# Kernel optimization log

Measured on AMD Instinct MI355X. Metric: run time of the kernel, lower is better.

## Reference

```python
import jax, jax.numpy as jnp
import numpy as np

N = 50000      # nodes (cells)
E = 800000     # directed edges
IN, H1, H2, Z = 512, 128, 128, 64


def setup_inputs() -> dict:
    key = jax.random.key(0)
    ks = jax.random.split(key, 12)
    x = jax.random.normal(ks[0], (N, IN), jnp.float32)
    edge_index = jax.random.randint(ks[1], (2, E), 0, N, dtype=jnp.int64)

    def glorot(k, i, o):
        return jax.random.normal(k, (i, o), jnp.float32) * np.float32(1.0 / np.sqrt(i))

    return {
        "x": x,
        "edge_index": edge_index,
        "W1": glorot(ks[2], IN, H1), "b1": jnp.zeros((H1,), jnp.float32),
        "W2": glorot(ks[3], H1, H2), "b2": jnp.zeros((H2,), jnp.float32),
        "Wm": glorot(ks[4], H2, Z),  "bm": jnp.zeros((Z,), jnp.float32),
        "Ws": glorot(ks[5], H2, Z),  "bs": jnp.zeros((Z,), jnp.float32),
    }


def _gcn_norm(edge_index, n):
    # PyG GCNConv default: add self-loops, sym-normalize D^-1/2 (A+I) D^-1/2
    loops = jnp.arange(n, dtype=edge_index.dtype)
    src = jnp.concatenate([edge_index[0], loops])
    dst = jnp.concatenate([edge_index[1], loops])
    deg = jax.ops.segment_sum(jnp.ones_like(dst, jnp.float32), dst, num_segments=n)
    dis = jnp.where(deg > 0, jax.lax.rsqrt(jnp.maximum(deg, 1.0)), 0.0)
    norm = dis[src] * dis[dst]  # [E+N]
    return src, dst, norm


def _gcn_conv(x, W, b, src, dst, norm, n):
    h = x @ W                          # [N, out] transform first
    msg = h[src] * norm[:, None]       # gather + scale
    out = jax.ops.segment_sum(msg, dst, num_segments=n)  # scatter-add at targets
    return out + b


def reference(x, edge_index, W1, b1, W2, b2, Wm, bm, Ws, bs):
    n = x.shape[0]
    src, dst, norm = _gcn_norm(edge_index, n)
    h = jax.nn.relu(_gcn_conv(x, W1, b1, src, dst, norm, n))
    h = jax.nn.relu(_gcn_conv(h, W2, b2, src, dst, norm, n))
    # dropout p=0.4 is identity in eval mode
    z_mean = _gcn_conv(h, Wm, bm, src, dst, norm, n)
    z_log_std = _gcn_conv(h, Ws, bs, src, dst, norm, n)
    return (z_mean, z_log_std)
```

## Files before the change

### kernel.cpp

```cpp
#include <hip/hip_runtime.h>


using u16 = unsigned short;
typedef __attribute__((ext_vector_type(8))) short short8;
typedef __attribute__((ext_vector_type(4))) float f32x4;

__device__ __forceinline__ void split_bf16(float f, u16& hi, u16& lo) {
    unsigned b = __float_as_uint(f);
    hi = (u16)(b >> 16);
    float rem = f - __uint_as_float(b & 0xFFFF0000u);
    lo = (u16)(__float_as_uint(rem) >> 16);
}

__device__ __forceinline__ int block_mode(const int* __restrict__ ew, int* sflag) {
    if (threadIdx.x == 0) *sflag = 0;
    __syncthreads();
    if (ew[2 * (int)threadIdx.x + 1] != 0) atomicOr(sflag, 1);
    __syncthreads();
    return *sflag ? 0 : 1;
}

__global__ void deg_kernel(const int* __restrict__ ew, int* __restrict__ deg, int E) {
    __shared__ int sflag;
    int mode = block_mode(ew, &sflag);
    int e = blockIdx.x * blockDim.x + threadIdx.x;
    if (e >= E) return;
    int d = mode ? ew[2 * E + 2 * e] : ew[E + e];
    atomicAdd(&deg[d], 1);
}

__global__ void scan_block_kernel(const int* __restrict__ deg, int* __restrict__ rowptr,
                                  int* __restrict__ aux, float* __restrict__ dis, int N) {
    __shared__ int s[256];
    int i = blockIdx.x * 256 + threadIdx.x;
    int v = (i < N) ? deg[i] : 0;
    if (i < N) dis[i] = rsqrtf((float)v + 1.0f);
    s[threadIdx.x] = v;
    __syncthreads();
    for (int off = 1; off < 256; off <<= 1) {
        int t = (threadIdx.x >= off) ? s[threadIdx.x - off] : 0;
        __syncthreads();
        s[threadIdx.x] += t;
        __syncthreads();
    }
    if (i < N) rowptr[i] = s[threadIdx.x] - v;
    if (threadIdx.x == 255) aux[blockIdx.x] = s[255];
}

__global__ void scan_aux_kernel(int* __restrict__ aux, int nb) {
    __shared__ int s[256];
    int i = threadIdx.x;
    int v = (i < nb) ? aux[i] : 0;
    s[i] = v;
    __syncthreads();
    for (int off = 1; off < 256; off <<= 1) {
        int t = (i >= off) ? s[i - off] : 0;
        __syncthreads();
        s[i] += t;
        __syncthreads();
    }
    if (i < nb) aux[i] = s[i] - v;
}

__global__ void add_offsets_kernel(int* __restrict__ rowptr, const int* __restrict__ aux,
                                   int N, int E) {
    int i = blockIdx.x * 256 + threadIdx.x;
    if (i < N) rowptr[i] += aux[i >> 8];
    if (i == 0) rowptr[N] = E;
}

__global__ void fill_csr_kernel(const int* __restrict__ ew,
                                const int* __restrict__ rowptr, int* __restrict__ cursor,
                                int* __restrict__ csr_src, int E) {
    __shared__ int sflag;
    int mode = block_mode(ew, &sflag);
    int e = blockIdx.x * blockDim.x + threadIdx.x;
    if (e >= E) return;
    int s = mode ? ew[2 * e] : ew[e];
    int d = mode ? ew[2 * E + 2 * e] : ew[E + e];
    int pos = rowptr[d] + atomicAdd(&cursor[d], 1);
    csr_src[pos] = s;
}

__global__ void conv_all_kernel(const float* __restrict__ W1, const float* __restrict__ W2,
                                const float* __restrict__ Wm, const float* __restrict__ Ws,
                                u16* __restrict__ W1t_hi, u16* __restrict__ W1t_lo,
                                u16* __restrict__ W2t_hi, u16* __restrict__ W2t_lo,
                                u16* __restrict__ Wct_hi, u16* __restrict__ Wct_lo) {
    int idx = blockIdx.x * 256 + threadIdx.x;
    u16 h, l;
    if (idx < 65536) {
        int k = idx >> 7, n = idx & 127;
        split_bf16(W1[idx], h, l);
        W1t_hi[n * 512 + k] = h;
        W1t_lo[n * 512 + k] = l;
    } else if (idx < 81920) {
        int t = idx - 65536;
        int k = t >> 7, n = t & 127;
        split_bf16(W2[t], h, l);
        W2t_hi[n * 128 + k] = h;
        W2t_lo[n * 128 + k] = l;
    } else if (idx < 98304) {
        int t = idx - 81920;
        int k = t >> 7, j = t & 127;
        float f = (j < 64) ? Wm[k * 64 + j] : Ws[k * 64 + (j - 64)];
        split_bf16(f, h, l);
        Wct_hi[j * 128 + k] = h;
        Wct_lo[j * 128 + k] = l;
    }
}

#define TILE_OFF(t) ((t) * 520)

__global__ __launch_bounds__(256) void gemm_mfma(const float* __restrict__ A,
                                                 const u16* __restrict__ Bt_hi,
                                                 const u16* __restrict__ Bt_lo,
                                                 float* __restrict__ C,
                                                 int N, int K) {
    __shared__ u16 AsH[4 * 520], AsL[4 * 520];
    __shared__ u16 BsH[8 * 520], BsL[8 * 520];

    const int tid = threadIdx.x;
    const int w = tid >> 6, lane = tid & 63;
    const int row0 = blockIdx.y * 64;

    const int s_ar = w * 16 + (lane & 15);
    const int s_ak = (lane >> 4) * 8;
    const int a_dst = TILE_OFF(w) + lane * 8;
    const int s_bc = tid >> 1;
    const int s_bk = (tid & 1) * 16;
    const int b_q0 = (tid & 1) * 2;
    const int b_dst0 = TILE_OFF(s_bc >> 4) + ((s_bc & 15) + 16 * (b_q0 + 0)) * 8;
    const int b_dst1 = TILE_OFF(s_bc >> 4) + ((s_bc & 15) + 16 * (b_q0 + 1)) * 8;

    const int R = (w >> 1) * 32, Cc = (w & 1) * 64;
    const int atile = (w >> 1) * 2;
    const int btile = (w & 1) * 4;
    const int m16 = lane & 15, quad = lane >> 4;

    f32x4 acc[2][4];
#pragma unroll
    for (int i = 0; i < 2; ++i)
#pragma unroll
        for (int j = 0; j < 4; ++j) acc[i][j] = (f32x4)0.f;

    const int grow = row0 + s_ar;
    const bool ok = (grow < N);
    const float* aptr = A + (size_t)grow * K + s_ak;
    const u16* bph = Bt_hi + (size_t)s_bc * K + s_bk;
    const u16* bpl = Bt_lo + (size_t)s_bc * K + s_bk;

    float av[8];
    short8 rbh0, rbh1, rbl0, rbl1;
    {
        f32x4 v0 = (f32x4)0.f, v1 = (f32x4)0.f;
        if (ok) { v0 = *(const f32x4*)&aptr[0]; v1 = *(const f32x4*)&aptr[4]; }
#pragma unroll
        for (int q = 0; q < 4; ++q) { av[q] = v0[q]; av[4 + q] = v1[q]; }
        rbh0 = *(const short8*)&bph[0];
        rbh1 = *(const short8*)&bph[8];
        rbl0 = *(const short8*)&bpl[0];
        rbl1 = *(const short8*)&bpl[8];
    }

    const int ksteps = K >> 5;
    for (int ks = 0; ks < ksteps; ++ks) {
        short8 ah, al;
#pragma unroll
        for (int q = 0; q < 8; ++q) {
            u16 h, l;
            split_bf16(av[q], h, l);
            ah[q] = (short)h;
            al[q] = (short)l;
        }
        __syncthreads();
        *(short8*)&AsH[a_dst] = ah;
        *(short8*)&AsL[a_dst] = al;
        *(short8*)&BsH[b_dst0] = rbh0;
        *(short8*)&BsH[b_dst1] = rbh1;
        *(short8*)&BsL[b_dst0] = rbl0;
        *(short8*)&BsL[b_dst1] = rbl1;
        __syncthreads();

        if (ks + 1 < ksteps) {
            const int k0 = (ks + 1) * 32;
            f32x4 v0 = (f32x4)0.f, v1 = (f32x4)0.f;
            if (ok) { v0 = *(const f32x4*)&aptr[k0]; v1 = *(const f32x4*)&aptr[k0 + 4]; }
#pragma unroll
            for (int q = 0; q < 4; ++q) { av[q] = v0[q]; av[4 + q] = v1[q]; }
            rbh0 = *(const short8*)&bph[k0];
            rbh1 = *(const short8*)&bph[k0 + 8];
            rbl0 = *(const short8*)&bpl[k0];
            rbl1 = *(const short8*)&bpl[k0 + 8];
        }

        short8 fa_h[2], fa_l[2], fb_h[4], fb_l[4];
#pragma unroll
        for (int i = 0; i < 2; ++i) {
            fa_h[i] = *(const short8*)&AsH[TILE_OFF(atile + i) + lane * 8];
            fa_l[i] = *(const short8*)&AsL[TILE_OFF(atile + i) + lane * 8];
        }
#pragma unroll
        for (int j = 0; j < 4; ++j) {
            fb_h[j] = *(const short8*)&BsH[TILE_OFF(btile + j) + lane * 8];
            fb_l[j] = *(const short8*)&BsL[TILE_OFF(btile + j) + lane * 8];
        }
#pragma unroll
        for (int i = 0; i < 2; ++i)
#pragma unroll
            for (int j = 0; j < 4; ++j) {
                acc[i][j] = __builtin_amdgcn_mfma_f32_16x16x32_bf16(
                    fa_h[i], fb_h[j], acc[i][j], 0, 0, 0);
                acc[i][j] = __builtin_amdgcn_mfma_f32_16x16x32_bf16(
                    fa_h[i], fb_l[j], acc[i][j], 0, 0, 0);
                acc[i][j] = __builtin_amdgcn_mfma_f32_16x16x32_bf16(
                    fa_l[i], fb_h[j], acc[i][j], 0, 0, 0);
            }
    }

#pragma unroll
    for (int i = 0; i < 2; ++i) {
#pragma unroll
        for (int r = 0; r < 4; ++r) {
            int gr = row0 + R + i * 16 + quad * 4 + r;
            if (gr < N) {
#pragma unroll
                for (int j = 0; j < 4; ++j)
                    C[(size_t)gr * 128 + Cc + j * 16 + m16] = acc[i][j][r];
            }
        }
    }
}

__global__ __launch_bounds__(256) void propagate_kernel(
    const float* __restrict__ h, const int* __restrict__ rowptr,
    const int* __restrict__ csr_src, const float* __restrict__ dis,
    const float* __restrict__ bias, float* __restrict__ out, int N, int do_relu) {
    int wave = (blockIdx.x * 256 + threadIdx.x) >> 6;
    int lane = threadIdx.x & 63;
    if (wave >= N) return;
    int v = wave;
    int f = lane * 2;
    float dv = dis[v];
    float ax = 0.f, ay = 0.f;
    int beg = rowptr[v], end = rowptr[v + 1];
    int i = beg;
    for (; i + 8 <= end; i += 8) {
        int s[8];
        float ww[8];
        float2 g[8];
#pragma unroll
        for (int u = 0; u < 8; ++u) s[u] = csr_src[i + u];
#pragma unroll
        for (int u = 0; u < 8; ++u) ww[u] = dis[s[u]];
#pragma unroll
        for (int u = 0; u < 8; ++u) g[u] = *(const float2*)&h[(size_t)s[u] * 128 + f];
#pragma unroll
        for (int u = 0; u < 8; ++u) {
            float t = ww[u] * dv;
            ax += t * g[u].x;
            ay += t * g[u].y;
        }
    }
    if (i + 4 <= end) {
        int s[4];
        float ww[4];
        float2 g[4];
#pragma unroll
        for (int u = 0; u < 4; ++u) s[u] = csr_src[i + u];
#pragma unroll
        for (int u = 0; u < 4; ++u) ww[u] = dis[s[u]];
#pragma unroll
        for (int u = 0; u < 4; ++u) g[u] = *(const float2*)&h[(size_t)s[u] * 128 + f];
#pragma unroll
        for (int u = 0; u < 4; ++u) {
            float t = ww[u] * dv;
            ax += t * g[u].x;
            ay += t * g[u].y;
        }
        i += 4;
    }
    for (; i < end; ++i) {
        int s = csr_src[i];
        float ws = dis[s] * dv;
        float2 g = *(const float2*)&h[(size_t)s * 128 + f];
        ax += ws * g.x;
        ay += ws * g.y;
    }
    float2 hv = *(const float2*)&h[(size_t)v * 128 + f];
    ax += dv * dv * hv.x;
    ay += dv * dv * hv.y;
    ax += bias[f];
    ay += bias[f + 1];
    if (do_relu) { ax = fmaxf(ax, 0.f); ay = fmaxf(ay, 0.f); }
    *(float2*)&out[(size_t)v * 128 + f] = make_float2(ax, ay);
}

__global__ __launch_bounds__(256) void propagate_final_kernel(
    const float* __restrict__ h, const int* __restrict__ rowptr,
    const int* __restrict__ csr_src, const float* __restrict__ dis,
    const float* __restrict__ bm, const float* __restrict__ bs,
    float* __restrict__ out, int N) {
    int wave = (blockIdx.x * 256 + threadIdx.x) >> 6;
    int lane = threadIdx.x & 63;
    if (wave >= N) return;
    int v = wave;
    int f = lane * 2;
    float dv = dis[v];
    float ax = 0.f, ay = 0.f;
    int beg = rowptr[v], end = rowptr[v + 1];
    int i = beg;
    for (; i + 8 <= end; i += 8) {
        int s[8];
        float ww[8];
        float2 g[8];
#pragma unroll
        for (int u = 0; u < 8; ++u) s[u] = csr_src[i + u];
#pragma unroll
        for (int u = 0; u < 8; ++u) ww[u] = dis[s[u]];
#pragma unroll
        for (int u = 0; u < 8; ++u) g[u] = *(const float2*)&h[(size_t)s[u] * 128 + f];
#pragma unroll
        for (int u = 0; u < 8; ++u) {
            float t = ww[u] * dv;
            ax += t * g[u].x;
            ay += t * g[u].y;
        }
    }
    if (i + 4 <= end) {
        int s[4];
        float ww[4];
        float2 g[4];
#pragma unroll
        for (int u = 0; u < 4; ++u) s[u] = csr_src[i + u];
#pragma unroll
        for (int u = 0; u < 4; ++u) ww[u] = dis[s[u]];
#pragma unroll
        for (int u = 0; u < 4; ++u) g[u] = *(const float2*)&h[(size_t)s[u] * 128 + f];
#pragma unroll
        for (int u = 0; u < 4; ++u) {
            float t = ww[u] * dv;
            ax += t * g[u].x;
            ay += t * g[u].y;
        }
        i += 4;
    }
    for (; i < end; ++i) {
        int s = csr_src[i];
        float ws = dis[s] * dv;
        float2 g = *(const float2*)&h[(size_t)s * 128 + f];
        ax += ws * g.x;
        ay += ws * g.y;
    }
    float2 hv = *(const float2*)&h[(size_t)v * 128 + f];
    ax += dv * dv * hv.x;
    ay += dv * dv * hv.y;
    if (f < 64) {
        *(float2*)&out[(size_t)v * 64 + f] = make_float2(ax + bm[f], ay + bm[f + 1]);
    } else {
        int g = f - 64;
        *(float2*)&out[(size_t)N * 64 + (size_t)v * 64 + g] =
            make_float2(ax + bs[g], ay + bs[g + 1]);
    }
}

extern "C" void kernel_launch(void* const* d_in, const int* in_sizes, int n_in,
                              void* d_out, int out_size, void* d_ws, size_t ws_size,
                              hipStream_t stream) {
    const float* x  = (const float*)d_in[0];
    const int*   ew = (const int*)d_in[1];
    const float* W1 = (const float*)d_in[2];
    const float* b1 = (const float*)d_in[3];
    const float* W2 = (const float*)d_in[4];
    const float* b2 = (const float*)d_in[5];
    const float* Wm = (const float*)d_in[6];
    const float* bm = (const float*)d_in[7];
    const float* Ws = (const float*)d_in[8];
    const float* bs = (const float*)d_in[9];
    float* out = (float*)d_out;

    const int IN = 512, H = 128;
    const int N = in_sizes[0] / IN;
    const int E = in_sizes[1] / 2;

    char* base = (char*)d_ws;
    size_t off = 0;
    auto alloc = [&](size_t bytes) -> char* {
        char* p = base + off;
        off = (off + bytes + 255) & ~(size_t)255;
        return p;
    };
    char*  degcur  = (char*) alloc(400384);
    float* dis     = (float*)alloc((size_t)N * 4);
    int*   rowptr  = (int*)  alloc((size_t)(N + 1) * 4);
    int*   aux     = (int*)  alloc(256 * 4);
    int*   csr_src = (int*)  alloc((size_t)E * 4);
    u16*   W1t_hi  = (u16*)  alloc((size_t)IN * H * 2);
    u16*   W1t_lo  = (u16*)  alloc((size_t)IN * H * 2);
    u16*   W2t_hi  = (u16*)  alloc((size_t)H * H * 2);
    u16*   W2t_lo  = (u16*)  alloc((size_t)H * H * 2);
    u16*   Wct_hi  = (u16*)  alloc((size_t)H * H * 2);
    u16*   Wct_lo  = (u16*)  alloc((size_t)H * H * 2);
    float* hA      = (float*)alloc((size_t)N * H * 4);
    float* hB      = (float*)alloc((size_t)N * H * 4);
    (void)ws_size; (void)n_in; (void)out_size;

    int* deg    = (int*)degcur;
    int* cursor = (int*)(degcur + 200192);

    hipMemsetAsync(degcur, 0, 400384, stream);

    const int eblocks = (E + 255) / 256;
    const int nblocks = (N + 255) / 256;

    conv_all_kernel<<<(98304 + 255) / 256, 256, 0, stream>>>(
        W1, W2, Wm, Ws, W1t_hi, W1t_lo, W2t_hi, W2t_lo, Wct_hi, Wct_lo);
    deg_kernel<<<eblocks, 256, 0, stream>>>(ew, deg, E);
    scan_block_kernel<<<nblocks, 256, 0, stream>>>(deg, rowptr, aux, dis, N);
    scan_aux_kernel<<<1, 256, 0, stream>>>(aux, nblocks);
    add_offsets_kernel<<<nblocks, 256, 0, stream>>>(rowptr, aux, N, E);
    fill_csr_kernel<<<eblocks, 256, 0, stream>>>(ew, rowptr, cursor, csr_src, E);

    dim3 gg(1, (N + 63) / 64);
    const int pblocks = (N * 64 + 255) / 256;

    gemm_mfma<<<gg, 256, 0, stream>>>(x, W1t_hi, W1t_lo, hA, N, IN);
    propagate_kernel<<<pblocks, 256, 0, stream>>>(hA, rowptr, csr_src, dis,
                                                  b1, hB, N, 1);
    gemm_mfma<<<gg, 256, 0, stream>>>(hB, W2t_hi, W2t_lo, hA, N, H);
    propagate_kernel<<<pblocks, 256, 0, stream>>>(hA, rowptr, csr_src, dis,
                                                  b2, hB, N, 1);
    gemm_mfma<<<gg, 256, 0, stream>>>(hB, Wct_hi, Wct_lo, hA, N, H);
    propagate_final_kernel<<<pblocks, 256, 0, stream>>>(hA, rowptr, csr_src, dis,
                                                        bm, bs, out, N);
}
```

Before: 499.5 us.

## Restructure propagation into feature slices, emit split bf16, fuse weight conversion with degree

The propagate kernels now give each block a 16-feature slice of 4 nodes, with four lane groups each walking a different subset of edges and combining partials by shuffle. This replaces the old scheme of one wave per node over all 128 features, aiming at better cache locality and memory parallelism. The hidden-layer propagate writes hi/lo bf16 splits directly, so the following GEMMs (templated on K and split mode) load pre-split A instead of converting fp32 in the inner loop. Weight conversion and degree counting are merged into one launch, and GEMM row indices are clamped instead of predicated. The risks are 8x more gather index and dis loads per node, and a scalar instead of float2 feature access.

```diff
diff --git a/kernel.cpp b/kernel.cpp
--- a/kernel.cpp
+++ b/kernel.cpp
@@ -20,13 +20,43 @@
     return *sflag ? 0 : 1;
 }
 
-__global__ void deg_kernel(const int* __restrict__ ew, int* __restrict__ deg, int E) {
-    __shared__ int sflag;
-    int mode = block_mode(ew, &sflag);
-    int e = blockIdx.x * blockDim.x + threadIdx.x;
-    if (e >= E) return;
-    int d = mode ? ew[2 * E + 2 * e] : ew[E + e];
-    atomicAdd(&deg[d], 1);
+#define CONVB 384
+__global__ void conv_deg_kernel(const float* __restrict__ W1, const float* __restrict__ W2,
+                                const float* __restrict__ Wm, const float* __restrict__ Ws,
+                                u16* __restrict__ W1t_hi, u16* __restrict__ W1t_lo,
+                                u16* __restrict__ W2t_hi, u16* __restrict__ W2t_lo,
+                                u16* __restrict__ Wct_hi, u16* __restrict__ Wct_lo,
+                                const int* __restrict__ ew, int* __restrict__ deg, int E) {
+    if (blockIdx.x < CONVB) {
+        int idx = blockIdx.x * 256 + threadIdx.x;
+        u16 h, l;
+        if (idx < 65536) {
+            int k = idx >> 7, n = idx & 127;
+            split_bf16(W1[idx], h, l);
+            W1t_hi[n * 512 + k] = h;
+            W1t_lo[n * 512 + k] = l;
+        } else if (idx < 81920) {
+            int t = idx - 65536;
+            int k = t >> 7, n = t & 127;
+            split_bf16(W2[t], h, l);
+            W2t_hi[n * 128 + k] = h;
+            W2t_lo[n * 128 + k] = l;
+        } else if (idx < 98304) {
+            int t = idx - 81920;
+            int k = t >> 7, j = t & 127;
+            float f = (j < 64) ? Wm[k * 64 + j] : Ws[k * 64 + (j - 64)];
+            split_bf16(f, h, l);
+            Wct_hi[j * 128 + k] = h;
+            Wct_lo[j * 128 + k] = l;
+        }
+    } else {
+        __shared__ int sflag;
+        int mode = block_mode(ew, &sflag);
+        int e = (blockIdx.x - CONVB) * 256 + threadIdx.x;
+        if (e >= E) return;
+        int d = mode ? ew[2 * E + 2 * e] : ew[E + e];
+        atomicAdd(&deg[d], 1);
+    }
 }
 
 __global__ void scan_block_kernel(const int* __restrict__ deg, int* __restrict__ rowptr,
@@ -82,47 +112,20 @@
     csr_src[pos] = s;
 }
 
-__global__ void conv_all_kernel(const float* __restrict__ W1, const float* __restrict__ W2,
-                                const float* __restrict__ Wm, const float* __restrict__ Ws,
-                                u16* __restrict__ W1t_hi, u16* __restrict__ W1t_lo,
-                                u16* __restrict__ W2t_hi, u16* __restrict__ W2t_lo,
-                                u16* __restrict__ Wct_hi, u16* __restrict__ Wct_lo) {
-    int idx = blockIdx.x * 256 + threadIdx.x;
-    u16 h, l;
-    if (idx < 65536) {
-        int k = idx >> 7, n = idx & 127;
-        split_bf16(W1[idx], h, l);
-        W1t_hi[n * 512 + k] = h;
-        W1t_lo[n * 512 + k] = l;
-    } else if (idx < 81920) {
-        int t = idx - 65536;
-        int k = t >> 7, n = t & 127;
-        split_bf16(W2[t], h, l);
-        W2t_hi[n * 128 + k] = h;
-        W2t_lo[n * 128 + k] = l;
-    } else if (idx < 98304) {
-        int t = idx - 81920;
-        int k = t >> 7, j = t & 127;
-        float f = (j < 64) ? Wm[k * 64 + j] : Ws[k * 64 + (j - 64)];
-        split_bf16(f, h, l);
-        Wct_hi[j * 128 + k] = h;
-        Wct_lo[j * 128 + k] = l;
-    }
-}
-
 #define TILE_OFF(t) ((t) * 520)
 
-__global__ __launch_bounds__(256) void gemm_mfma(const float* __restrict__ A,
-                                                 const u16* __restrict__ Bt_hi,
-                                                 const u16* __restrict__ Bt_lo,
-                                                 float* __restrict__ C,
-                                                 int N, int K) {
+template <int K, bool SPLIT>
+__global__ __launch_bounds__(256) void gemm_mfma(
+    const float* __restrict__ A,
+    const u16* __restrict__ Ahi, const u16* __restrict__ Alo,
+    const u16* __restrict__ Bh, const u16* __restrict__ Bl,
+    float* __restrict__ C, int N) {
     __shared__ u16 AsH[4 * 520], AsL[4 * 520];
     __shared__ u16 BsH[8 * 520], BsL[8 * 520];
 
     const int tid = threadIdx.x;
     const int w = tid >> 6, lane = tid & 63;
-    const int row0 = blockIdx.y * 64;
+    const int row0 = blockIdx.x * 64;
 
     const int s_ar = w * 16 + (lane & 15);
     const int s_ak = (lane >> 4) * 8;
@@ -144,19 +147,33 @@
 #pragma unroll
         for (int j = 0; j < 4; ++j) acc[i][j] = (f32x4)0.f;
 
-    const int grow = row0 + s_ar;
+    int grow = row0 + s_ar;
     const bool ok = (grow < N);
-    const float* aptr = A + (size_t)grow * K + s_ak;
-    const u16* bph = Bt_hi + (size_t)s_bc * K + s_bk;
-    const u16* bpl = Bt_lo + (size_t)s_bc * K + s_bk;
+    if (grow > N - 1) grow = N - 1;
+    const float* aptr;
+    const u16 *ahp, *alp;
+    if constexpr (SPLIT) {
+        ahp = Ahi + (size_t)grow * K + s_ak;
+        alp = Alo + (size_t)grow * K + s_ak;
+    } else {
+        aptr = A + (size_t)grow * K + s_ak;
+    }
+    const u16* bph = Bh + (size_t)s_bc * K + s_bk;
+    const u16* bpl = Bl + (size_t)s_bc * K + s_bk;
 
     float av[8];
+    short8 pah, pal;
     short8 rbh0, rbh1, rbl0, rbl1;
     {
-        f32x4 v0 = (f32x4)0.f, v1 = (f32x4)0.f;
-        if (ok) { v0 = *(const f32x4*)&aptr[0]; v1 = *(const f32x4*)&aptr[4]; }
-#pragma unroll
-        for (int q = 0; q < 4; ++q) { av[q] = v0[q]; av[4 + q] = v1[q]; }
+        if constexpr (SPLIT) {
+            pah = *(const short8*)&ahp[0];
+            pal = *(const short8*)&alp[0];
+        } else {
+            f32x4 v0 = (f32x4)0.f, v1 = (f32x4)0.f;
+            if (ok) { v0 = *(const f32x4*)&aptr[0]; v1 = *(const f32x4*)&aptr[4]; }
+#pragma unroll
+            for (int q = 0; q < 4; ++q) { av[q] = v0[q]; av[4 + q] = v1[q]; }
+        }
         rbh0 = *(const short8*)&bph[0];
         rbh1 = *(const short8*)&bph[8];
         rbl0 = *(const short8*)&bpl[0];
@@ -166,12 +183,16 @@
     const int ksteps = K >> 5;
     for (int ks = 0; ks < ksteps; ++ks) {
         short8 ah, al;
-#pragma unroll
-        for (int q = 0; q < 8; ++q) {
-            u16 h, l;
-            split_bf16(av[q], h, l);
-            ah[q] = (short)h;
-            al[q] = (short)l;
+        if constexpr (SPLIT) {
+            ah = pah; al = pal;
+        } else {
+#pragma unroll
+            for (int q = 0; q < 8; ++q) {
+                u16 h, l;
+                split_bf16(av[q], h, l);
+                ah[q] = (short)h;
+                al[q] = (short)l;
+            }
         }
         __syncthreads();
         *(short8*)&AsH[a_dst] = ah;
@@ -184,10 +205,15 @@
 
         if (ks + 1 < ksteps) {
             const int k0 = (ks + 1) * 32;
-            f32x4 v0 = (f32x4)0.f, v1 = (f32x4)0.f;
-            if (ok) { v0 = *(const f32x4*)&aptr[k0]; v1 = *(const f32x4*)&aptr[k0 + 4]; }
-#pragma unroll
-            for (int q = 0; q < 4; ++q) { av[q] = v0[q]; av[4 + q] = v1[q]; }
+            if constexpr (SPLIT) {
+                pah = *(const short8*)&ahp[k0];
+                pal = *(const short8*)&alp[k0];
+            } else {
+                f32x4 v0 = (f32x4)0.f, v1 = (f32x4)0.f;
+                if (ok) { v0 = *(const f32x4*)&aptr[k0]; v1 = *(const f32x4*)&aptr[k0 + 4]; }
+#pragma unroll
+                for (int q = 0; q < 4; ++q) { av[q] = v0[q]; av[4 + q] = v1[q]; }
+            }
             rbh0 = *(const short8*)&bph[k0];
             rbh1 = *(const short8*)&bph[k0 + 8];
             rbl0 = *(const short8*)&bpl[k0];
@@ -235,65 +261,45 @@
 __global__ __launch_bounds__(256) void propagate_kernel(
     const float* __restrict__ h, const int* __restrict__ rowptr,
     const int* __restrict__ csr_src, const float* __restrict__ dis,
-    const float* __restrict__ bias, float* __restrict__ out, int N, int do_relu) {
-    int wave = (blockIdx.x * 256 + threadIdx.x) >> 6;
-    int lane = threadIdx.x & 63;
-    if (wave >= N) return;
-    int v = wave;
-    int f = lane * 2;
-    float dv = dis[v];
-    float ax = 0.f, ay = 0.f;
-    int beg = rowptr[v], end = rowptr[v + 1];
-    int i = beg;
-    for (; i + 8 <= end; i += 8) {
-        int s[8];
-        float ww[8];
-        float2 g[8];
-#pragma unroll
-        for (int u = 0; u < 8; ++u) s[u] = csr_src[i + u];
-#pragma unroll
-        for (int u = 0; u < 8; ++u) ww[u] = dis[s[u]];
-#pragma unroll
-        for (int u = 0; u < 8; ++u) g[u] = *(const float2*)&h[(size_t)s[u] * 128 + f];
-#pragma unroll
-        for (int u = 0; u < 8; ++u) {
-            float t = ww[u] * dv;
-            ax += t * g[u].x;
-            ay += t * g[u].y;
-        }
-    }
-    if (i + 4 <= end) {
-        int s[4];
-        float ww[4];
-        float2 g[4];
-#pragma unroll
-        for (int u = 0; u < 4; ++u) s[u] = csr_src[i + u];
-#pragma unroll
-        for (int u = 0; u < 4; ++u) ww[u] = dis[s[u]];
-#pragma unroll
-        for (int u = 0; u < 4; ++u) g[u] = *(const float2*)&h[(size_t)s[u] * 128 + f];
-#pragma unroll
-        for (int u = 0; u < 4; ++u) {
-            float t = ww[u] * dv;
-            ax += t * g[u].x;
-            ay += t * g[u].y;
-        }
-        i += 4;
-    }
-    for (; i < end; ++i) {
-        int s = csr_src[i];
-        float ws = dis[s] * dv;
-        float2 g = *(const float2*)&h[(size_t)s * 128 + f];
-        ax += ws * g.x;
-        ay += ws * g.y;
-    }
-    float2 hv = *(const float2*)&h[(size_t)v * 128 + f];
-    ax += dv * dv * hv.x;
-    ay += dv * dv * hv.y;
-    ax += bias[f];
-    ay += bias[f + 1];
-    if (do_relu) { ax = fmaxf(ax, 0.f); ay = fmaxf(ay, 0.f); }
-    *(float2*)&out[(size_t)v * 128 + f] = make_float2(ax, ay);
+    const float* __restrict__ bias, u16* __restrict__ out_hi,
+    u16* __restrict__ out_lo, int N) {
+    const int slice = blockIdx.x & 7;
+    const int wave = threadIdx.x >> 6;
+    const int v = (blockIdx.x >> 3) * 4 + wave;
+    if (v >= N) return;
+    const int lane = threadIdx.x & 63;
+    const int g = lane >> 4;
+    const int f = slice * 16 + (lane & 15);
+    const float dv = dis[v];
+    const int beg = rowptr[v], end = rowptr[v + 1];
+    float acc = 0.f;
+    int i = beg + g;
+    for (; i + 4 < end; i += 8) {
+        int s0 = csr_src[i];
+        int s1 = csr_src[i + 4];
+        float w0 = dis[s0];
+        float w1 = dis[s1];
+        float g0 = h[(size_t)s0 * 128 + f];
+        float g1 = h[(size_t)s1 * 128 + f];
+        acc += w0 * g0;
+        acc += w1 * g1;
+    }
+    if (i < end) {
+        int s0 = csr_src[i];
+        acc += dis[s0] * h[(size_t)s0 * 128 + f];
+    }
+    acc += __shfl_down(acc, 32);
+    acc += __shfl_down(acc, 16);
+    if (g == 0) {
+        acc *= dv;
+        acc += dv * dv * h[(size_t)v * 128 + f];
+        acc += bias[f];
+        acc = fmaxf(acc, 0.f);
+        u16 hi, lo;
+        split_bf16(acc, hi, lo);
+        out_hi[(size_t)v * 128 + f] = hi;
+        out_lo[(size_t)v * 128 + f] = lo;
+    }
 }
 
 __global__ __launch_bounds__(256) void propagate_final_kernel(
@@ -301,66 +307,40 @@
     const int* __restrict__ csr_src, const float* __restrict__ dis,
     const float* __restrict__ bm, const float* __restrict__ bs,
     float* __restrict__ out, int N) {
-    int wave = (blockIdx.x * 256 + threadIdx.x) >> 6;
-    int lane = threadIdx.x & 63;
-    if (wave >= N) return;
-    int v = wave;
-    int f = lane * 2;
-    float dv = dis[v];
-    float ax = 0.f, ay = 0.f;
-    int beg = rowptr[v], end = rowptr[v + 1];
-    int i = beg;
-    for (; i + 8 <= end; i += 8) {
-        int s[8];
-        float ww[8];
-        float2 g[8];
-#pragma unroll
-        for (int u = 0; u < 8; ++u) s[u] = csr_src[i + u];
-#pragma unroll
-        for (int u = 0; u < 8; ++u) ww[u] = dis[s[u]];
-#pragma unroll
-        for (int u = 0; u < 8; ++u) g[u] = *(const float2*)&h[(size_t)s[u] * 128 + f];
-#pragma unroll
-        for (int u = 0; u < 8; ++u) {
-            float t = ww[u] * dv;
-            ax += t * g[u].x;
-            ay += t * g[u].y;
-        }
-    }
-    if (i + 4 <= end) {
-        int s[4];
-        float ww[4];
-        float2 g[4];
-#pragma unroll
-        for (int u = 0; u < 4; ++u) s[u] = csr_src[i + u];
-#pragma unroll
-        for (int u = 0; u < 4; ++u) ww[u] = dis[s[u]];
-#pragma unroll
-        for (int u = 0; u < 4; ++u) g[u] = *(const float2*)&h[(size_t)s[u] * 128 + f];
-#pragma unroll
-        for (int u = 0; u < 4; ++u) {
-            float t = ww[u] * dv;
-            ax += t * g[u].x;
-            ay += t * g[u].y;
-        }
-        i += 4;
-    }
-    for (; i < end; ++i) {
-        int s = csr_src[i];
-        float ws = dis[s] * dv;
-        float2 g = *(const float2*)&h[(size_t)s * 128 + f];
-        ax += ws * g.x;
-        ay += ws * g.y;
-    }
-    float2 hv = *(const float2*)&h[(size_t)v * 128 + f];
-    ax += dv * dv * hv.x;
-    ay += dv * dv * hv.y;
-    if (f < 64) {
-        *(float2*)&out[(size_t)v * 64 + f] = make_float2(ax + bm[f], ay + bm[f + 1]);
-    } else {
-        int g = f - 64;
-        *(float2*)&out[(size_t)N * 64 + (size_t)v * 64 + g] =
-            make_float2(ax + bs[g], ay + bs[g + 1]);
+    const int slice = blockIdx.x & 7;
+    const int wave = threadIdx.x >> 6;
+    const int v = (blockIdx.x >> 3) * 4 + wave;
+    if (v >= N) return;
+    const int lane = threadIdx.x & 63;
+    const int g = lane >> 4;
+    const int f = slice * 16 + (lane & 15);
+    const float dv = dis[v];
+    const int beg = rowptr[v], end = rowptr[v + 1];
+    float acc = 0.f;
+    int i = beg + g;
+    for (; i + 4 < end; i += 8) {
+        int s0 = csr_src[i];
+        int s1 = csr_src[i + 4];
+        float w0 = dis[s0];
+        float w1 = dis[s1];
+        float g0 = h[(size_t)s0 * 128 + f];
+        float g1 = h[(size_t)s1 * 128 + f];
+        acc += w0 * g0;
+        acc += w1 * g1;
+    }
+    if (i < end) {
+        int s0 = csr_src[i];
+        acc += dis[s0] * h[(size_t)s0 * 128 + f];
+    }
+    acc += __shfl_down(acc, 32);
+    acc += __shfl_down(acc, 16);
+    if (g == 0) {
+        acc *= dv;
+        acc += dv * dv * h[(size_t)v * 128 + f];
+        if (f < 64)
+            out[(size_t)v * 64 + f] = acc + bm[f];
+        else
+            out[(size_t)N * 64 + (size_t)v * 64 + (f - 64)] = acc + bs[f - 64];
     }
 }
 
@@ -402,7 +382,8 @@
     u16*   Wct_hi  = (u16*)  alloc((size_t)H * H * 2);
     u16*   Wct_lo  = (u16*)  alloc((size_t)H * H * 2);
     float* hA      = (float*)alloc((size_t)N * H * 4);
-    float* hB      = (float*)alloc((size_t)N * H * 4);
+    u16*   hBhi    = (u16*)  alloc((size_t)N * H * 2);
+    u16*   hBlo    = (u16*)  alloc((size_t)N * H * 2);
     (void)ws_size; (void)n_in; (void)out_size;
 
     int* deg    = (int*)degcur;
@@ -413,24 +394,27 @@
     const int eblocks = (E + 255) / 256;
     const int nblocks = (N + 255) / 256;
 
-    conv_all_kernel<<<(98304 + 255) / 256, 256, 0, stream>>>(
-        W1, W2, Wm, Ws, W1t_hi, W1t_lo, W2t_hi, W2t_lo, Wct_hi, Wct_lo);
-    deg_kernel<<<eblocks, 256, 0, stream>>>(ew, deg, E);
+    conv_deg_kernel<<<CONVB + eblocks, 256, 0, stream>>>(
+        W1, W2, Wm, Ws, W1t_hi, W1t_lo, W2t_hi, W2t_lo, Wct_hi, Wct_lo,
+        ew, deg, E);
     scan_block_kernel<<<nblocks, 256, 0, stream>>>(deg, rowptr, aux, dis, N);
     scan_aux_kernel<<<1, 256, 0, stream>>>(aux, nblocks);
     add_offsets_kernel<<<nblocks, 256, 0, stream>>>(rowptr, aux, N, E);
     fill_csr_kernel<<<eblocks, 256, 0, stream>>>(ew, rowptr, cursor, csr_src, E);
 
-    dim3 gg(1, (N + 63) / 64);
-    const int pblocks = (N * 64 + 255) / 256;
-
-    gemm_mfma<<<gg, 256, 0, stream>>>(x, W1t_hi, W1t_lo, hA, N, IN);
+    const int gblocks = (N + 63) / 64;
+    const int pblocks = ((N + 3) / 4) * 8;
+
+    gemm_mfma<512, false><<<gblocks, 256, 0, stream>>>(
+        x, nullptr, nullptr, W1t_hi, W1t_lo, hA, N);
     propagate_kernel<<<pblocks, 256, 0, stream>>>(hA, rowptr, csr_src, dis,
-                                                  b1, hB, N, 1);
-    gemm_mfma<<<gg, 256, 0, stream>>>(hB, W2t_hi, W2t_lo, hA, N, H);
+                                                  b1, hBhi, hBlo, N);
+    gemm_mfma<128, true><<<gblocks, 256, 0, stream>>>(
+        nullptr, hBhi, hBlo, W2t_hi, W2t_lo, hA, N);
     propagate_kernel<<<pblocks, 256, 0, stream>>>(hA, rowptr, csr_src, dis,
-                                                  b2, hB, N, 1);
-    gemm_mfma<<<gg, 256, 0, stream>>>(hB, Wct_hi, Wct_lo, hA, N, H);
+                                                  b2, hBhi, hBlo, N);
+    gemm_mfma<128, true><<<gblocks, 256, 0, stream>>>(
+        nullptr, hBhi, hBlo, Wct_hi, Wct_lo, hA, N);
     propagate_final_kernel<<<pblocks, 256, 0, stream>>>(hA, rowptr, csr_src, dis,
                                                         bm, bs, out, N);
 }
```

Result: slower. 790.6 us (+58.3%).
